# Kernel tuning notes

Hardware: AMD Instinct MI355X
Metric: run time of the kernel (lower is better)

## Reference

```python
import jax, jax.numpy as jnp
import numpy as np

B, T, E, H = 64, 577, 768, 64
GRID_H, GRID_W = 24, 24
NUM_PREFIX = 1
N = GRID_H * GRID_W  # 576 patches
EPS = 1e-5


def setup_inputs() -> dict:
    key = jax.random.key(0)
    ks = jax.random.split(key, 12)
    s = lambda k, shape, fan: jax.random.normal(k, shape, jnp.float32) / np.sqrt(fan)
    return {
        "x": jax.random.normal(ks[0], (B, T, E), jnp.float32),
        "w_q": s(ks[1], (E, H), E),
        "w_k": s(ks[2], (E, H), E),
        "w_v": s(ks[3], (E, H), E),
        "q_gamma": jnp.ones((H,), jnp.float32),
        "q_beta": jnp.zeros((H,), jnp.float32),
        "k_gamma": jnp.ones((H,), jnp.float32),
        "k_beta": jnp.zeros((H,), jnp.float32),
        "w_sigma": s(ks[4], (H, 2), H),
        "b_sigma": jnp.zeros((2,), jnp.float32),
        "w_alpha": s(ks[5], (H, 1), H),
        "b_alpha": jnp.zeros((1,), jnp.float32),
    }


def _layernorm(x, gamma, beta):
    mu = jnp.mean(x, axis=-1, keepdims=True)
    var = jnp.mean(jnp.square(x - mu), axis=-1, keepdims=True)
    return (x - mu) * jax.lax.rsqrt(var + EPS) * gamma + beta


def _grid_sq_dists():
    # coords[i] = (row, col) of patch i; squared coordinate differences [N, N]
    coords = jnp.stack(
        jnp.meshgrid(jnp.arange(GRID_H), jnp.arange(GRID_W), indexing="ij"), axis=-1
    ).reshape(N, 2).astype(jnp.float32)
    diff = coords[:, None, :] - coords[None, :, :]  # [N, N, 2]
    dy2 = jnp.square(diff[..., 0])  # row diff squared
    dx2 = jnp.square(diff[..., 1])  # col diff squared
    return dx2, dy2


def reference(x, w_q, w_k, w_v, q_gamma, q_beta, k_gamma, k_beta,
              w_sigma, b_sigma, w_alpha, b_alpha):
    q = _layernorm(x @ w_q, q_gamma, q_beta)  # [B, T, H]
    k = _layernorm(x @ w_k, k_gamma, k_beta)  # [B, T, H]
    v = x @ w_v                               # [B, T, H]

    sim = jnp.einsum("bqh,bkh->bqk", q, k)    # [B, T, T]

    q_nc = q[:, NUM_PREFIX:, :]               # [B, N, H]
    alpha = jax.nn.softplus(q_nc @ w_alpha + b_alpha)[..., 0]  # [B, N]
    sigma = jax.nn.sigmoid(q_nc @ w_sigma + b_sigma)           # [B, N, 2]
    sx = sigma[..., 0]  # [B, N]
    sy = sigma[..., 1]

    dx2, dy2 = _grid_sq_dists()  # [N, N] each
    # Gaussian decay bias: query-patch p controls sigma; [B, N, N]
    G = jnp.exp(
        -dx2[None] / (2.0 * jnp.square(sx)[:, :, None])
        - dy2[None] / (2.0 * jnp.square(sy)[:, :, None])
    )
    S = alpha[:, :, None] * G

    sim = sim.at[:, NUM_PREFIX:, NUM_PREFIX:].add(S)

    scale = jnp.sqrt(jnp.float32(H))
    attn = jax.nn.softmax(sim / scale, axis=-1)
    return attn @ v  # [B, T, H]
```

## Files before the change

### kernel.cpp

```cpp
#include <hip/hip_runtime.h>
#include <math.h>

#define B_ 64
#define T_ 577
#define E_ 768
#define H_ 64
#define N_ 576
#define GW_ 24

typedef float f32x4 __attribute__((ext_vector_type(4)));
typedef __bf16 bf16x8 __attribute__((ext_vector_type(8)));
typedef __bf16 bf16x4 __attribute__((ext_vector_type(4)));

__device__ inline void split_bf16(float f, __bf16& h, __bf16& l) {
  h = (__bf16)f;
  l = (__bf16)(f - (float)h);
}

__global__ __launch_bounds__(256) void prep_w_kernel(
    const float* __restrict__ wq, const float* __restrict__ wk, const float* __restrict__ wv,
    __bf16* __restrict__ wsw_hi, __bf16* __restrict__ wsw_lo)
{
  int t = blockIdx.x * 256 + threadIdx.x;
  if (t >= 24*192) return;
  int kc = t / 192, n = t - (t/192)*192;
  const float* src = (n < 64) ? wq : ((n < 128) ? wk : wv);
  int nn = n & 63;
  __bf16 hbuf[32], lbuf[32];
  #pragma unroll
  for (int kk = 0; kk < 32; ++kk) {
    float f = src[(size_t)(kc*32 + kk)*64 + nn];
    split_bf16(f, hbuf[kk], lbuf[kk]);
  }
  size_t base = (size_t)t * 32;
  #pragma unroll
  for (int i = 0; i < 4; ++i) {
    *(bf16x8*)(wsw_hi + base + i*8) = *(bf16x8*)&hbuf[i*8];
    *(bf16x8*)(wsw_lo + base + i*8) = *(bf16x8*)&lbuf[i*8];
  }
}

__global__ __launch_bounds__(256) void qkv_ln_kernel(
    const float* __restrict__ x,
    const __bf16* __restrict__ wsw_hi, const __bf16* __restrict__ wsw_lo,
    const float* __restrict__ qg, const float* __restrict__ qb,
    const float* __restrict__ kg, const float* __restrict__ kb,
    const float* __restrict__ wsig, const float* __restrict__ bsig,
    const float* __restrict__ walp, const float* __restrict__ balp,
    float* __restrict__ qo, float* __restrict__ ko, float* __restrict__ vo,
    float* __restrict__ alo, float* __restrict__ sxo, float* __restrict__ syo)
{
  __shared__ __align__(16) float smem[64*193 + 256];
  __bf16* A_hi = (__bf16*)smem;
  __bf16* A_lo = A_hi + 64*40;
  __bf16* B_hi = A_lo + 64*40;
  __bf16* B_lo = B_hi + 192*40;
  float (*Cs)[193] = (float (*)[193])smem;
  float* mu_q = smem + 64*193;
  float* rs_q = mu_q + 64;
  float* mu_k = rs_q + 64;
  float* rs_k = mu_k + 64;

  const int tid  = threadIdx.x;
  const int lane = tid & 63;
  const int w    = tid >> 6;
  const int rowbase = blockIdx.x << 6;

  f32x4 acc[4][3];
  #pragma unroll
  for (int mt = 0; mt < 4; ++mt)
    #pragma unroll
    for (int nt = 0; nt < 3; ++nt)
      acc[mt][nt] = (f32x4){0.f, 0.f, 0.f, 0.f};

  const int m     = lane & 15;
  const int kfrag = (lane >> 4) * 8;

  float4 xr0, xr1;
  bf16x8 whr[3], wlr[3];
  const int s0 = tid, s1 = tid + 256;
  const int arow0 = s0 >> 3, ak0 = (s0 & 7) * 4;
  const int arow1 = s1 >> 3, ak1 = (s1 & 7) * 4;

  auto load_chunk = [&](int kc) {
    xr0 = *(const float4*)(x + (size_t)(rowbase + arow0)*E_ + kc*32 + ak0);
    xr1 = *(const float4*)(x + (size_t)(rowbase + arow1)*E_ + kc*32 + ak1);
    #pragma unroll
    for (int i = 0; i < 3; ++i) {
      int e = tid + 256*i;
      whr[i] = *(const bf16x8*)(wsw_hi + (size_t)kc*6144 + e*8);
      wlr[i] = *(const bf16x8*)(wsw_lo + (size_t)kc*6144 + e*8);
    }
  };
  auto store_chunk = [&]() {
    __bf16 h0,l0,h1,l1,h2,l2,h3,l3;
    split_bf16(xr0.x,h0,l0); split_bf16(xr0.y,h1,l1);
    split_bf16(xr0.z,h2,l2); split_bf16(xr0.w,h3,l3);
    *(bf16x4*)&A_hi[arow0*40 + ak0] = (bf16x4){h0,h1,h2,h3};
    *(bf16x4*)&A_lo[arow0*40 + ak0] = (bf16x4){l0,l1,l2,l3};
    split_bf16(xr1.x,h0,l0); split_bf16(xr1.y,h1,l1);
    split_bf16(xr1.z,h2,l2); split_bf16(xr1.w,h3,l3);
    *(bf16x4*)&A_hi[arow1*40 + ak1] = (bf16x4){h0,h1,h2,h3};
    *(bf16x4*)&A_lo[arow1*40 + ak1] = (bf16x4){l0,l1,l2,l3};
    #pragma unroll
    for (int i = 0; i < 3; ++i) {
      int e = tid + 256*i;
      int n = e >> 2, g = e & 3;
      *(bf16x8*)&B_hi[n*40 + g*8] = whr[i];
      *(bf16x8*)&B_lo[n*40 + g*8] = wlr[i];
    }
  };

  load_chunk(0);
  #pragma unroll 1
  for (int kc = 0; kc < 24; ++kc) {
    __syncthreads();
    store_chunk();
    __syncthreads();
    if (kc < 23) load_chunk(kc + 1);

    bf16x8 bh[3], bl[3];
    #pragma unroll
    for (int nt = 0; nt < 3; ++nt) {
      int n = w*48 + nt*16 + m;
      bh[nt] = *(const bf16x8*)&B_hi[n*40 + kfrag];
      bl[nt] = *(const bf16x8*)&B_lo[n*40 + kfrag];
    }
    #pragma unroll
    for (int mt = 0; mt < 4; ++mt) {
      bf16x8 ah = *(const bf16x8*)&A_hi[(mt*16 + m)*40 + kfrag];
      bf16x8 al = *(const bf16x8*)&A_lo[(mt*16 + m)*40 + kfrag];
      #pragma unroll
      for (int nt = 0; nt < 3; ++nt) {
        acc[mt][nt] = __builtin_amdgcn_mfma_f32_16x16x32_bf16(ah, bh[nt], acc[mt][nt], 0, 0, 0);
        acc[mt][nt] = __builtin_amdgcn_mfma_f32_16x16x32_bf16(al, bh[nt], acc[mt][nt], 0, 0, 0);
        acc[mt][nt] = __builtin_amdgcn_mfma_f32_16x16x32_bf16(ah, bl[nt], acc[mt][nt], 0, 0, 0);
      }
    }
  }
  __syncthreads();

  #pragma unroll
  for (int mt = 0; mt < 4; ++mt)
    #pragma unroll
    for (int nt = 0; nt < 3; ++nt) {
      int row = mt*16 + (lane >> 4)*4;
      int col = w*48 + nt*16 + (lane & 15);
      Cs[row + 0][col] = acc[mt][nt].x;
      Cs[row + 1][col] = acc[mt][nt].y;
      Cs[row + 2][col] = acc[mt][nt].z;
      Cs[row + 3][col] = acc[mt][nt].w;
    }
  __syncthreads();

  if (tid < 64) {
    float s = 0.f;
    for (int h = 0; h < 64; ++h) s += Cs[tid][h];
    float mu = s * (1.f/64.f);
    float vs = 0.f;
    for (int h = 0; h < 64; ++h) { float d = Cs[tid][h] - mu; vs += d*d; }
    mu_q[tid] = mu;
    rs_q[tid] = rsqrtf(vs*(1.f/64.f) + 1e-5f);
  } else if (tid < 128) {
    int r = tid - 64;
    float s = 0.f;
    for (int h = 0; h < 64; ++h) s += Cs[r][64+h];
    float mu = s * (1.f/64.f);
    float vs = 0.f;
    for (int h = 0; h < 64; ++h) { float d = Cs[r][64+h] - mu; vs += d*d; }
    mu_k[r] = mu;
    rs_k[r] = rsqrtf(vs*(1.f/64.f) + 1e-5f);
  }
  __syncthreads();

  if (tid >= 192) {
    int r = tid - 192;
    int mrow = rowbase + r;
    int tindex = mrow % T_;
    if (tindex >= 1) {
      int bb = mrow / T_;
      int g = tindex - 1;
      float mu = mu_q[r], rs = rs_q[r];
      float za = 0.f, z0 = 0.f, z1 = 0.f;
      for (int h = 0; h < 64; ++h) {
        float qv = (Cs[r][h] - mu) * rs * qg[h] + qb[h];
        za += qv * walp[h];
        z0 += qv * wsig[2*h];
        z1 += qv * wsig[2*h+1];
      }
      za += balp[0]; z0 += bsig[0]; z1 += bsig[1];
      float al = fmaxf(za, 0.f) + log1pf(__expf(-fabsf(za)));
      float sx = 1.f/(1.f + __expf(-z0));
      float sy = 1.f/(1.f + __expf(-z1));
      alo[bb*N_ + g] = al;
      sxo[bb*N_ + g] = 0.5f/(sx*sx);
      syo[bb*N_ + g] = 0.5f/(sy*sy);
    }
  }
  for (int idx = tid; idx < 64*48; idx += 256) {
    int r = idx / 48, c4 = (idx - (idx/48)*48) * 4;
    size_t row = (size_t)rowbase + r;
    float4 val = make_float4(Cs[r][c4], Cs[r][c4+1], Cs[r][c4+2], Cs[r][c4+3]);
    if (c4 < 64) {
      float mu = mu_q[r], rs = rs_q[r];
      float4 o;
      o.x = (val.x - mu)*rs*qg[c4+0] + qb[c4+0];
      o.y = (val.y - mu)*rs*qg[c4+1] + qb[c4+1];
      o.z = (val.z - mu)*rs*qg[c4+2] + qb[c4+2];
      o.w = (val.w - mu)*rs*qg[c4+3] + qb[c4+3];
      *(float4*)(qo + row*64 + c4) = o;
    } else if (c4 < 128) {
      int h = c4 - 64;
      float mu = mu_k[r], rs = rs_k[r];
      float4 o;
      o.x = (val.x - mu)*rs*kg[h+0] + kb[h+0];
      o.y = (val.y - mu)*rs*kg[h+1] + kb[h+1];
      o.z = (val.z - mu)*rs*kg[h+2] + kb[h+2];
      o.w = (val.w - mu)*rs*kg[h+3] + kb[h+3];
      *(float4*)(ko + row*64 + h) = o;
    } else {
      *(float4*)(vo + row*64 + (c4-128)) = val;
    }
  }
}

__global__ __launch_bounds__(256) void attn_kernel(
    const float* __restrict__ q, const float* __restrict__ k, const float* __restrict__ v,
    const float* __restrict__ ala, const float* __restrict__ sxa, const float* __restrict__ sya,
    float* __restrict__ out)
{
  __shared__ __align__(16) __bf16 sm[8*4608];
  __shared__ float prm_al[64], prm_sx[64], prm_sy[64], prm_gr[64], prm_gc[64];
  __shared__ int   prm_has[64];

  __bf16* QH = sm;            __bf16* QL = sm + 4608;
  __bf16* KH = sm + 2*4608;   __bf16* KL = sm + 3*4608;
  __bf16* VH = sm + 4*4608;   __bf16* VL = sm + 5*4608;
  __bf16* PH = sm + 6*4608;   __bf16* PL = sm + 7*4608;

  const int tid  = threadIdx.x;
  const int lane = tid & 63;
  const int w    = tid >> 6;
  const int quad = lane >> 4;
  const int mrow = lane & 15;
  const int b    = blockIdx.y;
  const int qt   = blockIdx.x;

  const float* qbase = q + (size_t)b * T_ * H_;
  const float* kbase = k + (size_t)b * T_ * H_;
  const float* vbase = v + (size_t)b * T_ * H_;

  if (tid < 64) {
    int row = qt*64 + tid;
    float al=0.f, isx=0.f, isy=0.f, gr=0.f, gc=0.f; int has = 0;
    if (row >= 1 && row < T_) {
      int g = row - 1;
      al  = ala[b*N_ + g] * 0.125f;
      isx = sxa[b*N_ + g];
      isy = sya[b*N_ + g];
      gr  = (float)(g / GW_);
      gc  = (float)(g - (g/GW_)*GW_);
      has = 1;
    }
    prm_al[tid]=al; prm_sx[tid]=isx; prm_sy[tid]=isy;
    prm_gr[tid]=gr; prm_gc[tid]=gc; prm_has[tid]=has;
  }
  #pragma unroll
  for (int i = 0; i < 4; ++i) {
    int s = tid + 256*i;
    int r = s >> 4, c4 = (s & 15)*4;
    int row = qt*64 + r;
    int rowc = row < T_ ? row : T_ - 1;
    float4 v4 = *(const float4*)(qbase + (size_t)rowc*H_ + c4);
    v4.x *= 0.125f; v4.y *= 0.125f; v4.z *= 0.125f; v4.w *= 0.125f;
    __bf16 h0,l0,h1,l1,h2,l2,h3,l3;
    split_bf16(v4.x,h0,l0); split_bf16(v4.y,h1,l1);
    split_bf16(v4.z,h2,l2); split_bf16(v4.w,h3,l3);
    *(bf16x4*)&QH[r*72 + c4] = (bf16x4){h0,h1,h2,h3};
    *(bf16x4*)&QL[r*72 + c4] = (bf16x4){l0,l1,l2,l3};
  }
  __syncthreads();

  float p_al[4], p_sx[4], p_sy[4], p_gr[4], p_gc[4]; int p_has[4];
  #pragma unroll
  for (int reg = 0; reg < 4; ++reg) {
    int rr = w*16 + quad*4 + reg;
    p_al[reg]=prm_al[rr]; p_sx[reg]=prm_sx[rr]; p_sy[reg]=prm_sy[rr];
    p_gr[reg]=prm_gr[rr]; p_gc[reg]=prm_gc[rr]; p_has[reg]=prm_has[rr];
  }

  float mo[4], lsum[4], O_[4][4];
  #pragma unroll
  for (int reg = 0; reg < 4; ++reg) { mo[reg] = -INFINITY; lsum[reg] = 0.f; }
  #pragma unroll
  for (int nt = 0; nt < 4; ++nt)
    #pragma unroll
    for (int reg = 0; reg < 4; ++reg) O_[nt][reg] = 0.f;

  float4 kreg[4];
  float  vreg[16];
  const int d0 = tid & 15, k0 = (tid >> 4) * 4;

  auto load_kv = [&](int kt) {
    #pragma unroll
    for (int i = 0; i < 4; ++i) {
      int s = tid + 256*i;
      int key = s >> 4, c4 = (s & 15)*4;
      int kgl = kt*64 + key;
      int kcl = kgl < T_ ? kgl : T_ - 1;
      kreg[i] = *(const float4*)(kbase + (size_t)kcl*H_ + c4);
    }
    #pragma unroll
    for (int di = 0; di < 4; ++di)
      #pragma unroll
      for (int ki = 0; ki < 4; ++ki) {
        int kgl = kt*64 + k0 + ki;
        int kcl = kgl < T_ ? kgl : T_ - 1;
        vreg[di*4+ki] = vbase[(size_t)kcl*H_ + d0 + 16*di];
      }
  };
  auto store_kv = [&]() {
    #pragma unroll
    for (int i = 0; i < 4; ++i) {
      int s = tid + 256*i;
      int key = s >> 4, c4 = (s & 15)*4;
      __bf16 h0,l0,h1,l1,h2,l2,h3,l3;
      split_bf16(kreg[i].x,h0,l0); split_bf16(kreg[i].y,h1,l1);
      split_bf16(kreg[i].z,h2,l2); split_bf16(kreg[i].w,h3,l3);
      *(bf16x4*)&KH[key*72 + c4] = (bf16x4){h0,h1,h2,h3};
      *(bf16x4*)&KL[key*72 + c4] = (bf16x4){l0,l1,l2,l3};
    }
    #pragma unroll
    for (int di = 0; di < 4; ++di) {
      int dim = d0 + 16*di;
      __bf16 h0,l0,h1,l1,h2,l2,h3,l3;
      split_bf16(vreg[di*4+0],h0,l0); split_bf16(vreg[di*4+1],h1,l1);
      split_bf16(vreg[di*4+2],h2,l2); split_bf16(vreg[di*4+3],h3,l3);
      *(bf16x4*)&VH[dim*72 + k0] = (bf16x4){h0,h1,h2,h3};
      *(bf16x4*)&VL[dim*72 + k0] = (bf16x4){l0,l1,l2,l3};
    }
  };

  load_kv(0);
  #pragma unroll 1
  for (int kt = 0; kt < 10; ++kt) {
    __syncthreads();
    store_kv();
    __syncthreads();
    if (kt < 9) load_kv(kt + 1);

    float S_[4][4];
    {
      f32x4 sac[4];
      #pragma unroll
      for (int nt = 0; nt < 4; ++nt) sac[nt] = (f32x4){0.f,0.f,0.f,0.f};
      #pragma unroll
      for (int ks = 0; ks < 2; ++ks) {
        int ko_ = ks*32 + quad*8;
        bf16x8 qh = *(const bf16x8*)&QH[(w*16 + mrow)*72 + ko_];
        bf16x8 ql = *(const bf16x8*)&QL[(w*16 + mrow)*72 + ko_];
        #pragma unroll
        for (int nt = 0; nt < 4; ++nt) {
          bf16x8 kh = *(const bf16x8*)&KH[(nt*16 + mrow)*72 + ko_];
          bf16x8 kl = *(const bf16x8*)&KL[(nt*16 + mrow)*72 + ko_];
          sac[nt] = __builtin_amdgcn_mfma_f32_16x16x32_bf16(qh, kh, sac[nt], 0, 0, 0);
          sac[nt] = __builtin_amdgcn_mfma_f32_16x16x32_bf16(ql, kh, sac[nt], 0, 0, 0);
          sac[nt] = __builtin_amdgcn_mfma_f32_16x16x32_bf16(qh, kl, sac[nt], 0, 0, 0);
        }
      }
      #pragma unroll
      for (int nt = 0; nt < 4; ++nt) {
        S_[nt][0] = sac[nt].x; S_[nt][1] = sac[nt].y;
        S_[nt][2] = sac[nt].z; S_[nt][3] = sac[nt].w;
      }
    }

    #pragma unroll
    for (int nt = 0; nt < 4; ++nt) {
      int keyg = kt*64 + nt*16 + mrow;
      bool kval = keyg < T_;
      bool khas = (keyg >= 1) && kval;
      float kgf = (float)(keyg - 1);
      float krf = floorf(kgf * (1.0f/24.0f));
      float kcf = kgf - 24.f*krf;
      #pragma unroll
      for (int reg = 0; reg < 4; ++reg) {
        float sval = S_[nt][reg];
        float dx = p_gc[reg] - kcf, dy = p_gr[reg] - krf;
        float bias = p_al[reg] * __expf(-(dx*dx*p_sx[reg] + dy*dy*p_sy[reg]));
        sval += (khas && p_has[reg]) ? bias : 0.f;
        S_[nt][reg] = kval ? sval : -1e30f;
      }
    }

    float lt_[4], sc_[4], mn_[4];
    #pragma unroll
    for (int reg = 0; reg < 4; ++reg) {
      float mx = fmaxf(fmaxf(S_[0][reg], S_[1][reg]), fmaxf(S_[2][reg], S_[3][reg]));
      mx = fmaxf(mx, __shfl_xor(mx, 1, 64));
      mx = fmaxf(mx, __shfl_xor(mx, 2, 64));
      mx = fmaxf(mx, __shfl_xor(mx, 4, 64));
      mx = fmaxf(mx, __shfl_xor(mx, 8, 64));
      mn_[reg] = fmaxf(mo[reg], mx);
      lt_[reg] = 0.f;
    }
    #pragma unroll
    for (int nt = 0; nt < 4; ++nt)
      #pragma unroll
      for (int reg = 0; reg < 4; ++reg) {
        float p = __expf(S_[nt][reg] - mn_[reg]);
        S_[nt][reg] = p;
        lt_[reg] += p;
      }
    #pragma unroll
    for (int reg = 0; reg < 4; ++reg) {
      float ls = lt_[reg];
      ls += __shfl_xor(ls, 1, 64);
      ls += __shfl_xor(ls, 2, 64);
      ls += __shfl_xor(ls, 4, 64);
      ls += __shfl_xor(ls, 8, 64);
      sc_[reg] = __expf(mo[reg] - mn_[reg]);
      lsum[reg] = lsum[reg]*sc_[reg] + ls;
      mo[reg] = mn_[reg];
    }
    #pragma unroll
    for (int nt = 0; nt < 4; ++nt)
      #pragma unroll
      for (int reg = 0; reg < 4; ++reg) O_[nt][reg] *= sc_[reg];

    #pragma unroll
    for (int nt = 0; nt < 4; ++nt)
      #pragma unroll
      for (int reg = 0; reg < 4; ++reg) {
        float p = S_[nt][reg];
        __bf16 ph, pl;
        split_bf16(p, ph, pl);
        int addr = (w*16 + quad*4 + reg)*72 + nt*16 + mrow;
        PH[addr] = ph;
        PL[addr] = pl;
      }

    #pragma unroll
    for (int nt = 0; nt < 4; ++nt) {
      f32x4 c = (f32x4){O_[nt][0], O_[nt][1], O_[nt][2], O_[nt][3]};
      #pragma unroll
      for (int ks = 0; ks < 2; ++ks) {
        int ko_ = ks*32 + quad*8;
        bf16x8 pah  = *(const bf16x8*)&PH[(w*16 + mrow)*72 + ko_];
        bf16x8 pall = *(const bf16x8*)&PL[(w*16 + mrow)*72 + ko_];
        bf16x8 vh   = *(const bf16x8*)&VH[(nt*16 + mrow)*72 + ko_];
        bf16x8 vl   = *(const bf16x8*)&VL[(nt*16 + mrow)*72 + ko_];
        c = __builtin_amdgcn_mfma_f32_16x16x32_bf16(pah, vh, c, 0, 0, 0);
        c = __builtin_amdgcn_mfma_f32_16x16x32_bf16(pall, vh, c, 0, 0, 0);
        c = __builtin_amdgcn_mfma_f32_16x16x32_bf16(pah, vl, c, 0, 0, 0);
      }
      O_[nt][0] = c.x; O_[nt][1] = c.y; O_[nt][2] = c.z; O_[nt][3] = c.w;
    }
  }

  #pragma unroll
  for (int reg = 0; reg < 4; ++reg) {
    int rowg = qt*64 + w*16 + quad*4 + reg;
    if (rowg < T_) {
      float inv = 1.f / lsum[reg];
      #pragma unroll
      for (int nt = 0; nt < 4; ++nt) {
        out[((size_t)b*T_ + rowg)*H_ + nt*16 + mrow] = O_[nt][reg] * inv;
      }
    }
  }
}

extern "C" void kernel_launch(void* const* d_in, const int* in_sizes, int n_in,
                              void* d_out, int out_size, void* d_ws, size_t ws_size,
                              hipStream_t stream) {
  const float* x      = (const float*)d_in[0];
  const float* wq     = (const float*)d_in[1];
  const float* wk     = (const float*)d_in[2];
  const float* wv     = (const float*)d_in[3];
  const float* qg     = (const float*)d_in[4];
  const float* qb     = (const float*)d_in[5];
  const float* kg     = (const float*)d_in[6];
  const float* kb     = (const float*)d_in[7];
  const float* wsig   = (const float*)d_in[8];
  const float* bsig   = (const float*)d_in[9];
  const float* walp   = (const float*)d_in[10];
  const float* balp   = (const float*)d_in[11];
  float* out = (float*)d_out;

  float* ws  = (float*)d_ws;
  const size_t nrow = (size_t)B_ * T_;
  float* qo  = ws;
  float* ko  = qo + nrow*H_;
  float* vo  = ko + nrow*H_;
  float* alo = vo + nrow*H_;
  float* sxo = alo + (size_t)B_*N_;
  float* syo = sxo + (size_t)B_*N_;
  __bf16* wsw_hi = (__bf16*)(syo + (size_t)B_*N_);
  __bf16* wsw_lo = wsw_hi + 24*192*32;

  hipLaunchKernelGGL(prep_w_kernel, dim3(18), dim3(256), 0, stream,
                     wq, wk, wv, wsw_hi, wsw_lo);
  hipLaunchKernelGGL(qkv_ln_kernel, dim3(577), dim3(256), 0, stream,
                     x, wsw_hi, wsw_lo, qg, qb, kg, kb, wsig, bsig, walp, balp,
                     qo, ko, vo, alo, sxo, syo);
  hipLaunchKernelGGL(attn_kernel, dim3(10, B_), dim3(256), 0, stream,
                     qo, ko, vo, alo, sxo, syo, out);
}
```

Measured before the change: 289.4 us.

## Read weight fragments from global, double-buffer x loads, shrink attention LDS

```diff
diff --git a/kernel.cpp b/kernel.cpp
--- a/kernel.cpp
+++ b/kernel.cpp
@@ -12,7 +12,7 @@
 typedef __bf16 bf16x8 __attribute__((ext_vector_type(8)));
 typedef __bf16 bf16x4 __attribute__((ext_vector_type(4)));
 
-__device__ inline void split_bf16(float f, __bf16& h, __bf16& l) {
+__device__ __forceinline__ void split_bf16(float f, __bf16& h, __bf16& l) {
   h = (__bf16)f;
   l = (__bf16)(f - (float)h);
 }
@@ -40,7 +40,7 @@
   }
 }
 
-__global__ __launch_bounds__(256) void qkv_ln_kernel(
+__global__ __launch_bounds__(256, 3) void qkv_kernel(
     const float* __restrict__ x,
     const __bf16* __restrict__ wsw_hi, const __bf16* __restrict__ wsw_lo,
     const float* __restrict__ qg, const float* __restrict__ qb,
@@ -53,8 +53,6 @@
   __shared__ __align__(16) float smem[64*193 + 256];
   __bf16* A_hi = (__bf16*)smem;
   __bf16* A_lo = A_hi + 64*40;
-  __bf16* B_hi = A_lo + 64*40;
-  __bf16* B_lo = B_hi + 192*40;
   float (*Cs)[193] = (float (*)[193])smem;
   float* mu_q = smem + 64*193;
   float* rs_q = mu_q + 64;
@@ -76,56 +74,42 @@
   const int m     = lane & 15;
   const int kfrag = (lane >> 4) * 8;
 
-  float4 xr0, xr1;
-  bf16x8 whr[3], wlr[3];
-  const int s0 = tid, s1 = tid + 256;
-  const int arow0 = s0 >> 3, ak0 = (s0 & 7) * 4;
-  const int arow1 = s1 >> 3, ak1 = (s1 & 7) * 4;
-
-  auto load_chunk = [&](int kc) {
-    xr0 = *(const float4*)(x + (size_t)(rowbase + arow0)*E_ + kc*32 + ak0);
-    xr1 = *(const float4*)(x + (size_t)(rowbase + arow1)*E_ + kc*32 + ak1);
-    #pragma unroll
-    for (int i = 0; i < 3; ++i) {
-      int e = tid + 256*i;
-      whr[i] = *(const bf16x8*)(wsw_hi + (size_t)kc*6144 + e*8);
-      wlr[i] = *(const bf16x8*)(wsw_lo + (size_t)kc*6144 + e*8);
-    }
-  };
-  auto store_chunk = [&]() {
+  const int arow0 = tid >> 3,         ak0 = (tid & 7) * 4;
+  const int arow1 = (tid + 256) >> 3, ak1 = (tid & 7) * 4;
+
+  float4 xA0, xA1, xB0, xB1;
+
+  auto loadA_A = [&](int kc) {
+    int c = kc > 23 ? 23 : kc;
+    xA0 = *(const float4*)(x + (size_t)(rowbase + arow0)*E_ + c*32 + ak0);
+    xA1 = *(const float4*)(x + (size_t)(rowbase + arow1)*E_ + c*32 + ak1);
+  };
+  auto loadA_B = [&](int kc) {
+    int c = kc > 23 ? 23 : kc;
+    xB0 = *(const float4*)(x + (size_t)(rowbase + arow0)*E_ + c*32 + ak0);
+    xB1 = *(const float4*)(x + (size_t)(rowbase + arow1)*E_ + c*32 + ak1);
+  };
+  auto storeA = [&](float4 r0, float4 r1) {
     __bf16 h0,l0,h1,l1,h2,l2,h3,l3;
-    split_bf16(xr0.x,h0,l0); split_bf16(xr0.y,h1,l1);
-    split_bf16(xr0.z,h2,l2); split_bf16(xr0.w,h3,l3);
+    split_bf16(r0.x,h0,l0); split_bf16(r0.y,h1,l1);
+    split_bf16(r0.z,h2,l2); split_bf16(r0.w,h3,l3);
     *(bf16x4*)&A_hi[arow0*40 + ak0] = (bf16x4){h0,h1,h2,h3};
     *(bf16x4*)&A_lo[arow0*40 + ak0] = (bf16x4){l0,l1,l2,l3};
-    split_bf16(xr1.x,h0,l0); split_bf16(xr1.y,h1,l1);
-    split_bf16(xr1.z,h2,l2); split_bf16(xr1.w,h3,l3);
+    split_bf16(r1.x,h0,l0); split_bf16(r1.y,h1,l1);
+    split_bf16(r1.z,h2,l2); split_bf16(r1.w,h3,l3);
     *(bf16x4*)&A_hi[arow1*40 + ak1] = (bf16x4){h0,h1,h2,h3};
     *(bf16x4*)&A_lo[arow1*40 + ak1] = (bf16x4){l0,l1,l2,l3};
-    #pragma unroll
-    for (int i = 0; i < 3; ++i) {
-      int e = tid + 256*i;
-      int n = e >> 2, g = e & 3;
-      *(bf16x8*)&B_hi[n*40 + g*8] = whr[i];
-      *(bf16x8*)&B_lo[n*40 + g*8] = wlr[i];
-    }
-  };
-
-  load_chunk(0);
-  #pragma unroll 1
-  for (int kc = 0; kc < 24; ++kc) {
-    __syncthreads();
-    store_chunk();
-    __syncthreads();
-    if (kc < 23) load_chunk(kc + 1);
-
-    bf16x8 bh[3], bl[3];
+  };
+  auto loadB = [&](int kc, bf16x8* bh, bf16x8* bl) {
+    int c = kc > 23 ? 23 : kc;
     #pragma unroll
     for (int nt = 0; nt < 3; ++nt) {
-      int n = w*48 + nt*16 + m;
-      bh[nt] = *(const bf16x8*)&B_hi[n*40 + kfrag];
-      bl[nt] = *(const bf16x8*)&B_lo[n*40 + kfrag];
-    }
+      size_t off = (size_t)c*6144 + (size_t)(w*48 + nt*16 + m)*32 + kfrag;
+      bh[nt] = *(const bf16x8*)(wsw_hi + off);
+      bl[nt] = *(const bf16x8*)(wsw_lo + off);
+    }
+  };
+  auto mfma_step = [&](bf16x8* bh, bf16x8* bl) {
     #pragma unroll
     for (int mt = 0; mt < 4; ++mt) {
       bf16x8 ah = *(const bf16x8*)&A_hi[(mt*16 + m)*40 + kfrag];
@@ -137,6 +121,28 @@
         acc[mt][nt] = __builtin_amdgcn_mfma_f32_16x16x32_bf16(ah, bl[nt], acc[mt][nt], 0, 0, 0);
       }
     }
+  };
+
+  bf16x8 bhC[3], blC[3], bhN[3], blN[3];
+  loadA_A(0);
+  loadA_B(1);
+  loadB(0, bhC, blC);
+
+  #pragma unroll 1
+  for (int kc2 = 0; kc2 < 12; ++kc2) {
+    int kc = kc2 * 2;
+    __syncthreads();
+    storeA(xA0, xA1);
+    __syncthreads();
+    loadA_A(kc + 2);
+    loadB(kc + 1, bhN, blN);
+    mfma_step(bhC, blC);
+    __syncthreads();
+    storeA(xB0, xB1);
+    __syncthreads();
+    loadA_B(kc + 3);
+    loadB(kc + 2, bhC, blC);
+    mfma_step(bhN, blN);
   }
   __syncthreads();
 
@@ -224,27 +230,32 @@
   }
 }
 
-__global__ __launch_bounds__(256) void attn_kernel(
+#define PAD_ 68
+__global__ __launch_bounds__(256, 3) void attn_kernel(
     const float* __restrict__ q, const float* __restrict__ k, const float* __restrict__ v,
     const float* __restrict__ ala, const float* __restrict__ sxa, const float* __restrict__ sya,
     float* __restrict__ out)
 {
-  __shared__ __align__(16) __bf16 sm[8*4608];
-  __shared__ float prm_al[64], prm_sx[64], prm_sy[64], prm_gr[64], prm_gc[64];
-  __shared__ int   prm_has[64];
-
-  __bf16* QH = sm;            __bf16* QL = sm + 4608;
-  __bf16* KH = sm + 2*4608;   __bf16* KL = sm + 3*4608;
-  __bf16* VH = sm + 4*4608;   __bf16* VL = sm + 5*4608;
-  __bf16* PH = sm + 6*4608;   __bf16* PL = sm + 7*4608;
+  __shared__ __align__(16) char smraw[6*8704 + 1536];
+  __bf16* sm = (__bf16*)smraw;
+  __bf16* QH = sm;            __bf16* QL = sm + 4352;
+  __bf16* KH = sm + 2*4352;   __bf16* KL = sm + 3*4352;
+  __bf16* VH = sm + 4*4352;   __bf16* VL = sm + 5*4352;
+  __bf16* PH = KH;            __bf16* PL = KL;
+  float* prm_al = (float*)(smraw + 6*8704);
+  float* prm_sx = prm_al + 64;
+  float* prm_sy = prm_sx + 64;
+  float* prm_gr = prm_sy + 64;
+  float* prm_gc = prm_gr + 64;
+  int*   prm_has = (int*)(prm_gc + 64);
 
   const int tid  = threadIdx.x;
   const int lane = tid & 63;
   const int w    = tid >> 6;
   const int quad = lane >> 4;
   const int mrow = lane & 15;
-  const int b    = blockIdx.y;
-  const int qt   = blockIdx.x;
+  const int b    = blockIdx.x / 10;
+  const int qt   = blockIdx.x - b*10;
 
   const float* qbase = q + (size_t)b * T_ * H_;
   const float* kbase = k + (size_t)b * T_ * H_;
@@ -276,8 +287,8 @@
     __bf16 h0,l0,h1,l1,h2,l2,h3,l3;
     split_bf16(v4.x,h0,l0); split_bf16(v4.y,h1,l1);
     split_bf16(v4.z,h2,l2); split_bf16(v4.w,h3,l3);
-    *(bf16x4*)&QH[r*72 + c4] = (bf16x4){h0,h1,h2,h3};
-    *(bf16x4*)&QL[r*72 + c4] = (bf16x4){l0,l1,l2,l3};
+    *(bf16x4*)&QH[r*PAD_ + c4] = (bf16x4){h0,h1,h2,h3};
+    *(bf16x4*)&QL[r*PAD_ + c4] = (bf16x4){l0,l1,l2,l3};
   }
   __syncthreads();
 
@@ -327,8 +338,8 @@
       __bf16 h0,l0,h1,l1,h2,l2,h3,l3;
       split_bf16(kreg[i].x,h0,l0); split_bf16(kreg[i].y,h1,l1);
       split_bf16(kreg[i].z,h2,l2); split_bf16(kreg[i].w,h3,l3);
-      *(bf16x4*)&KH[key*72 + c4] = (bf16x4){h0,h1,h2,h3};
-      *(bf16x4*)&KL[key*72 + c4] = (bf16x4){l0,l1,l2,l3};
+      *(bf16x4*)&KH[key*PAD_ + c4] = (bf16x4){h0,h1,h2,h3};
+      *(bf16x4*)&KL[key*PAD_ + c4] = (bf16x4){l0,l1,l2,l3};
     }
     #pragma unroll
     for (int di = 0; di < 4; ++di) {
@@ -336,8 +347,8 @@
       __bf16 h0,l0,h1,l1,h2,l2,h3,l3;
       split_bf16(vreg[di*4+0],h0,l0); split_bf16(vreg[di*4+1],h1,l1);
       split_bf16(vreg[di*4+2],h2,l2); split_bf16(vreg[di*4+3],h3,l3);
-      *(bf16x4*)&VH[dim*72 + k0] = (bf16x4){h0,h1,h2,h3};
-      *(bf16x4*)&VL[dim*72 + k0] = (bf16x4){l0,l1,l2,l3};
+      *(bf16x4*)&VH[dim*PAD_ + k0] = (bf16x4){h0,h1,h2,h3};
+      *(bf16x4*)&VL[dim*PAD_ + k0] = (bf16x4){l0,l1,l2,l3};
     }
   };
 
@@ -357,12 +368,12 @@
       #pragma unroll
       for (int ks = 0; ks < 2; ++ks) {
         int ko_ = ks*32 + quad*8;
-        bf16x8 qh = *(const bf16x8*)&QH[(w*16 + mrow)*72 + ko_];
-        bf16x8 ql = *(const bf16x8*)&QL[(w*16 + mrow)*72 + ko_];
+        bf16x8 qh = *(const bf16x8*)&QH[(w*16 + mrow)*PAD_ + ko_];
+        bf16x8 ql = *(const bf16x8*)&QL[(w*16 + mrow)*PAD_ + ko_];
         #pragma unroll
         for (int nt = 0; nt < 4; ++nt) {
-          bf16x8 kh = *(const bf16x8*)&KH[(nt*16 + mrow)*72 + ko_];
-          bf16x8 kl = *(const bf16x8*)&KL[(nt*16 + mrow)*72 + ko_];
+          bf16x8 kh = *(const bf16x8*)&KH[(nt*16 + mrow)*PAD_ + ko_];
+          bf16x8 kl = *(const bf16x8*)&KL[(nt*16 + mrow)*PAD_ + ko_];
           sac[nt] = __builtin_amdgcn_mfma_f32_16x16x32_bf16(qh, kh, sac[nt], 0, 0, 0);
           sac[nt] = __builtin_amdgcn_mfma_f32_16x16x32_bf16(ql, kh, sac[nt], 0, 0, 0);
           sac[nt] = __builtin_amdgcn_mfma_f32_16x16x32_bf16(qh, kl, sac[nt], 0, 0, 0);
@@ -374,6 +385,7 @@
         S_[nt][2] = sac[nt].z; S_[nt][3] = sac[nt].w;
       }
     }
+    __syncthreads();
 
     #pragma unroll
     for (int nt = 0; nt < 4; ++nt) {
@@ -435,7 +447,7 @@
         float p = S_[nt][reg];
         __bf16 ph, pl;
         split_bf16(p, ph, pl);
-        int addr = (w*16 + quad*4 + reg)*72 + nt*16 + mrow;
+        int addr = (w*16 + quad*4 + reg)*PAD_ + nt*16 + mrow;
         PH[addr] = ph;
         PL[addr] = pl;
       }
@@ -446,10 +458,10 @@
       #pragma unroll
       for (int ks = 0; ks < 2; ++ks) {
         int ko_ = ks*32 + quad*8;
-        bf16x8 pah  = *(const bf16x8*)&PH[(w*16 + mrow)*72 + ko_];
-        bf16x8 pall = *(const bf16x8*)&PL[(w*16 + mrow)*72 + ko_];
-        bf16x8 vh   = *(const bf16x8*)&VH[(nt*16 + mrow)*72 + ko_];
-        bf16x8 vl   = *(const bf16x8*)&VL[(nt*16 + mrow)*72 + ko_];
+        bf16x8 pah  = *(const bf16x8*)&PH[(w*16 + mrow)*PAD_ + ko_];
+        bf16x8 pall = *(const bf16x8*)&PL[(w*16 + mrow)*PAD_ + ko_];
+        bf16x8 vh   = *(const bf16x8*)&VH[(nt*16 + mrow)*PAD_ + ko_];
+        bf16x8 vl   = *(const bf16x8*)&VL[(nt*16 + mrow)*PAD_ + ko_];
         c = __builtin_amdgcn_mfma_f32_16x16x32_bf16(pah, vh, c, 0, 0, 0);
         c = __builtin_amdgcn_mfma_f32_16x16x32_bf16(pall, vh, c, 0, 0, 0);
         c = __builtin_amdgcn_mfma_f32_16x16x32_bf16(pah, vl, c, 0, 0, 0);
@@ -501,9 +513,9 @@
 
   hipLaunchKernelGGL(prep_w_kernel, dim3(18), dim3(256), 0, stream,
                      wq, wk, wv, wsw_hi, wsw_lo);
-  hipLaunchKernelGGL(qkv_ln_kernel, dim3(577), dim3(256), 0, stream,
+  hipLaunchKernelGGL(qkv_kernel, dim3(577), dim3(256), 0, stream,
                      x, wsw_hi, wsw_lo, qg, qb, kg, kb, wsig, bsig, walp, balp,
                      qo, ko, vo, alo, sxo, syo);
-  hipLaunchKernelGGL(attn_kernel, dim3(10, B_), dim3(256), 0, stream,
+  hipLaunchKernelGGL(attn_kernel, dim3(640), dim3(256), 0, stream,
                      qo, ko, vo, alo, sxo, syo, out);
 }
```

New measurement: 384.0 us. +32.7%, slower.
